# Kernel tuning notes

Measured on AMD Instinct MI355X. Metric: run time of the kernel, lower is better.

The kernel has to match this reference:

```python
import jax, jax.numpy as jnp
import numpy as np

D_MODEL = 1024
N_HEADS = 16
CHUNK_LEN = 50
MEM_LEN = 16
TOTAL_PROB = 20000
TOTAL_SKILL = 1000
B = 64
L = 2000
EPS = 1e-5


def _layernorm(x, g, b):
    mu = jnp.mean(x, axis=-1, keepdims=True)
    var = jnp.var(x, axis=-1, keepdims=True)
    return (x - mu) * jax.lax.rsqrt(var + EPS) * g + b


def setup_inputs() -> dict:
    key = jax.random.key(0)
    ks = jax.random.split(key, 20)
    s = 0.02
    D = D_MODEL
    emb_problem = (jax.random.normal(ks[0], (TOTAL_PROB, D), jnp.float32) * s).at[0].set(0.0)  # padding_idx=0
    emb_skill = (jax.random.normal(ks[1], (TOTAL_SKILL, D), jnp.float32) * s).at[0].set(0.0)
    mem_init = jax.random.normal(ks[2], (1, MEM_LEN, D), jnp.float32) * s
    pos_emb = jax.random.normal(ks[3], (MEM_LEN + CHUNK_LEN, D), jnp.float32) * s
    w_qkv = jax.random.normal(ks[4], (3 * D, D), jnp.float32) * s
    b_qkv = jnp.zeros((3 * D,), jnp.float32)
    w_out = jax.random.normal(ks[5], (D, D), jnp.float32) * s
    b_out = jnp.zeros((D,), jnp.float32)
    w1 = jax.random.normal(ks[6], (4 * D, D), jnp.float32) * s
    b1 = jnp.zeros((4 * D,), jnp.float32)
    w2 = jax.random.normal(ks[7], (D, 4 * D), jnp.float32) * s
    b2 = jnp.zeros((D,), jnp.float32)
    g_attn = jnp.ones((D,), jnp.float32)
    be_attn = jnp.zeros((D,), jnp.float32)
    g_ffn = jnp.ones((D,), jnp.float32)
    be_ffn = jnp.zeros((D,), jnp.float32)
    w_gate = jax.random.normal(ks[8], (D, D), jnp.float32) * s
    b_gate = jnp.zeros((D,), jnp.float32)
    in_prob = jax.random.randint(ks[9], (B, L), 0, TOTAL_PROB, dtype=jnp.int64 if jax.config.jax_enable_x64 else jnp.int32)
    in_skill = jax.random.randint(ks[10], (B, L), 0, TOTAL_SKILL, dtype=jnp.int64 if jax.config.jax_enable_x64 else jnp.int32)
    return dict(in_prob=in_prob, in_skill=in_skill, emb_problem=emb_problem, emb_skill=emb_skill,
                mem_init=mem_init, pos_emb=pos_emb, w_qkv=w_qkv, b_qkv=b_qkv, w_out=w_out, b_out=b_out,
                w1=w1, b1=b1, w2=w2, b2=b2, g_attn=g_attn, be_attn=be_attn, g_ffn=g_ffn, be_ffn=be_ffn,
                w_gate=w_gate, b_gate=b_gate)


def _mha(z, w_qkv, b_qkv, w_out, b_out, mask):
    # z: [B, T, D]; mask: [T, T] bool, True = disallowed (torch attn_mask semantics)
    Bz, T, D = z.shape
    dh = D // N_HEADS
    qkv = z @ w_qkv.T + b_qkv  # [B, T, 3D]
    q, k, v = jnp.split(qkv, 3, axis=-1)
    def heads(x):
        return x.reshape(Bz, T, N_HEADS, dh).transpose(0, 2, 1, 3)  # [B, H, T, dh]
    q, k, v = heads(q), heads(k), heads(v)
    scores = jnp.einsum('bhqd,bhkd->bhqk', q, k) / jnp.sqrt(jnp.float32(dh))
    scores = jnp.where(mask[None, None], jnp.float32(-1e9), scores)
    a = jax.nn.softmax(scores, axis=-1)
    o = jnp.einsum('bhqk,bhkd->bhqd', a, v)  # [B, H, T, dh]
    o = o.transpose(0, 2, 1, 3).reshape(Bz, T, D)
    return o @ w_out.T + b_out


def reference(in_prob, in_skill, emb_problem, emb_skill, mem_init, pos_emb,
              w_qkv, b_qkv, w_out, b_out, w1, b1, w2, b2,
              g_attn, be_attn, g_ffn, be_ffn, w_gate, b_gate):
    Bx, Lx = in_prob.shape
    D = emb_problem.shape[1]
    x = emb_problem[in_prob] + emb_skill[in_skill]  # [B, L, D]
    n_chunks = Lx // CHUNK_LEN
    T = MEM_LEN + CHUNK_LEN
    # block mask: memory fully visible, chunk part strictly causal
    causal = jnp.triu(jnp.ones((CHUNK_LEN, CHUNK_LEN), bool), k=1)
    mask = jnp.zeros((T, T), bool).at[MEM_LEN:, MEM_LEN:].set(causal)
    pos = pos_emb[:T][None]  # [1, T, D]
    chunks = x.reshape(Bx, n_chunks, CHUNK_LEN, D).transpose(1, 0, 2, 3)  # [K, B, Lc, D]
    mem0 = jnp.broadcast_to(mem_init, (Bx, MEM_LEN, D))

    def step(mem, xs):
        chunk, kidx = xs
        z = jnp.concatenate([mem, chunk], axis=1) + pos  # [B, T, D]
        z = z + _mha(_layernorm(z, g_attn, be_attn), w_qkv, b_qkv, w_out, b_out, mask)
        h = _layernorm(z, g_ffn, be_ffn)
        z = z + (jax.nn.relu(h @ w1.T + b1) @ w2.T + b2)
        mem_cand = z[:, :MEM_LEN]
        h_k = z[:, MEM_LEN:]
        g = jax.nn.sigmoid(mem_cand @ w_gate.T + b_gate)
        mem_gated = g * mem_cand + (1.0 - g) * mem
        mem_new = jnp.where(kidx == 0, mem_cand, mem_gated)  # first chunk: no gate
        return mem_new, h_k

    mem_final, hs = jax.lax.scan(step, mem0, (chunks, jnp.arange(n_chunks)))
    enc_out = hs.transpose(1, 0, 2, 3).reshape(Bx, Lx, D)
    return enc_out, mem_final
```

## Files before the change

### kernel.cpp

```cpp
#include <hip/hip_runtime.h>
#include <hip/hip_bf16.h>

#define D_MODEL 1024
#define N_HEADS 16
#define DH 64
#define CHUNK_LEN 50
#define MEM_LEN 16
#define TT 66
#define BB 64
#define LL 2000
#define NCHUNK 40
#define MTOK (BB*TT)

typedef _Float16 half8_t __attribute__((ext_vector_type(8)));
typedef __attribute__((ext_vector_type(4))) float f32x4;

typedef __attribute__((address_space(1))) const void GVoid;
typedef __attribute__((address_space(3))) void LVoid;

__device__ __forceinline__ void gload16(const void* g, void* l) {
  __builtin_amdgcn_global_load_lds((GVoid*)g, (LVoid*)l, 16, 0, 0);
}

__global__ __launch_bounds__(256) void f2h_kernel(const float* __restrict__ in,
                                                  _Float16* __restrict__ out, int n) {
  int i = (blockIdx.x * 256 + threadIdx.x) * 4;
  if (i < n) {
    float4 v = *(const float4*)(in + i);
    out[i+0] = (_Float16)v.x;
    out[i+1] = (_Float16)v.y;
    out[i+2] = (_Float16)v.z;
    out[i+3] = (_Float16)v.w;
  }
}

__global__ __launch_bounds__(256) void build_z_ln(
    const int* __restrict__ in_prob, const int* __restrict__ in_skill,
    const float* __restrict__ emb_p, const float* __restrict__ emb_s,
    const float* __restrict__ mem_src, int mem_bstride,
    const float* __restrict__ pos,
    const float* __restrict__ gam, const float* __restrict__ bet,
    float* __restrict__ z, _Float16* __restrict__ zn, int chunk)
{
  int row = blockIdx.x;
  int b = row / TT, t = row % TT;
  int tid = threadIdx.x;
  int d = tid * 4;
  float4 v;
  if (t < MEM_LEN) {
    v = *(const float4*)(mem_src + (size_t)b*mem_bstride + t*D_MODEL + d);
  } else {
    int tok = chunk*CHUNK_LEN + (t - MEM_LEN);
    int p = in_prob[b*LL + tok];
    int s = in_skill[b*LL + tok];
    float4 vp = *(const float4*)(emb_p + (size_t)p*D_MODEL + d);
    float4 vs = *(const float4*)(emb_s + (size_t)s*D_MODEL + d);
    v = make_float4(vp.x+vs.x, vp.y+vs.y, vp.z+vs.z, vp.w+vs.w);
  }
  float4 pv = *(const float4*)(pos + t*D_MODEL + d);
  v.x += pv.x; v.y += pv.y; v.z += pv.z; v.w += pv.w;
  *(float4*)(z + (size_t)row*D_MODEL + d) = v;
  float sum = v.x+v.y+v.z+v.w;
  float sq  = v.x*v.x+v.y*v.y+v.z*v.z+v.w*v.w;
  #pragma unroll
  for (int off = 32; off; off >>= 1) {
    sum += __shfl_down(sum, off, 64);
    sq  += __shfl_down(sq,  off, 64);
  }
  __shared__ float rs_[4], rq_[4];
  int wave = tid >> 6, lane = tid & 63;
  if (lane == 0) { rs_[wave] = sum; rq_[wave] = sq; }
  __syncthreads();
  sum = rs_[0]+rs_[1]+rs_[2]+rs_[3];
  sq  = rq_[0]+rq_[1]+rq_[2]+rq_[3];
  float mu  = sum * (1.0f/D_MODEL);
  float var = sq  * (1.0f/D_MODEL) - mu*mu;
  float rstd = rsqrtf(var + 1e-5f);
  float4 gv = *(const float4*)(gam + d);
  float4 bv = *(const float4*)(bet + d);
  _Float16* o = zn + (size_t)row*D_MODEL + d;
  o[0] = (_Float16)((v.x-mu)*rstd*gv.x + bv.x);
  o[1] = (_Float16)((v.y-mu)*rstd*gv.y + bv.y);
  o[2] = (_Float16)((v.z-mu)*rstd*gv.z + bv.z);
  o[3] = (_Float16)((v.w-mu)*rstd*gv.w + bv.w);
}

__global__ __launch_bounds__(256) void ln_kernel(
    const float* __restrict__ z, const float* __restrict__ gam, const float* __restrict__ bet,
    _Float16* __restrict__ out)
{
  int row = blockIdx.x;
  int tid = threadIdx.x;
  int d = tid * 4;
  float4 v = *(const float4*)(z + (size_t)row*D_MODEL + d);
  float sum = v.x+v.y+v.z+v.w;
  float sq  = v.x*v.x+v.y*v.y+v.z*v.z+v.w*v.w;
  #pragma unroll
  for (int off = 32; off; off >>= 1) {
    sum += __shfl_down(sum, off, 64);
    sq  += __shfl_down(sq,  off, 64);
  }
  __shared__ float rs_[4], rq_[4];
  int wave = tid >> 6, lane = tid & 63;
  if (lane == 0) { rs_[wave] = sum; rq_[wave] = sq; }
  __syncthreads();
  sum = rs_[0]+rs_[1]+rs_[2]+rs_[3];
  sq  = rq_[0]+rq_[1]+rq_[2]+rq_[3];
  float mu  = sum * (1.0f/D_MODEL);
  float var = sq  * (1.0f/D_MODEL) - mu*mu;
  float rstd = rsqrtf(var + 1e-5f);
  float4 gv = *(const float4*)(gam + d);
  float4 bv = *(const float4*)(bet + d);
  _Float16* o = out + (size_t)row*D_MODEL + d;
  o[0] = (_Float16)((v.x-mu)*rstd*gv.x + bv.x);
  o[1] = (_Float16)((v.y-mu)*rstd*gv.y + bv.y);
  o[2] = (_Float16)((v.z-mu)*rstd*gv.z + bv.z);
  o[3] = (_Float16)((v.w-mu)*rstd*gv.w + bv.w);
}

__global__ __launch_bounds__(256) void attn_kernel(
    const _Float16* __restrict__ qkv, _Float16* __restrict__ attn_o)
{
  __shared__ float qs_t[64*68 + 8];
  __shared__ float ks_t[64*68 + 8];
  __shared__ float vs[TT*DH];
  __shared__ float sc[TT*67];
  int bh = blockIdx.x; int b = bh >> 4, h = bh & 15;
  int tid = threadIdx.x;
  const _Float16* base = qkv + (size_t)b*TT*3072 + h*DH;
  for (int i = tid; i < TT*DH; i += 256) {
    int t = i >> 6, d2 = i & 63;
    const _Float16* rp = base + (size_t)t*3072 + d2;
    qs_t[d2*68 + t] = (float)rp[0];
    ks_t[d2*68 + t] = (float)rp[1024];
    vs[t*64 + d2]   = (float)rp[2048];
  }
  __syncthreads();
  if (tid < 153) {
    int ti = tid / 9, tj = tid % 9;
    int qi0 = ti*4, kj0 = tj*8;
    float acc[4][8];
    #pragma unroll
    for (int i = 0; i < 4; i++)
      #pragma unroll
      for (int j = 0; j < 8; j++) acc[i][j] = 0.f;
    for (int d2 = 0; d2 < 64; d2++) {
      float4 qv = *(const float4*)(qs_t + d2*68 + qi0);
      float4 k0 = *(const float4*)(ks_t + d2*68 + kj0);
      float4 k1 = *(const float4*)(ks_t + d2*68 + kj0 + 4);
      float q_[4] = {qv.x, qv.y, qv.z, qv.w};
      float k_[8] = {k0.x, k0.y, k0.z, k0.w, k1.x, k1.y, k1.z, k1.w};
      #pragma unroll
      for (int i = 0; i < 4; i++)
        #pragma unroll
        for (int j = 0; j < 8; j++)
          acc[i][j] += q_[i]*k_[j];
    }
    #pragma unroll
    for (int i = 0; i < 4; i++) {
      int qi = qi0 + i;
      if (qi >= TT) continue;
      #pragma unroll
      for (int j = 0; j < 8; j++) {
        int kj = kj0 + j;
        if (kj >= TT) continue;
        float s;
        if (qi >= MEM_LEN && kj >= MEM_LEN && kj > qi) s = -1e9f;
        else s = acc[i][j]*0.125f;
        sc[qi*67 + kj] = s;
      }
    }
  }
  __syncthreads();
  if (tid < TT) {
    float* r = sc + tid*67;
    float m = -1e30f;
    for (int j = 0; j < TT; j++) m = fmaxf(m, r[j]);
    float ssum = 0.f;
    for (int j = 0; j < TT; j++) { float e = __expf(r[j]-m); r[j] = e; ssum += e; }
    float inv = 1.f/ssum;
    for (int j = 0; j < TT; j++) r[j] *= inv;
  }
  __syncthreads();
  if (tid < 136) {
    int ti = tid >> 3, tj = tid & 7;
    int qi0 = ti*4, d20 = tj*8;
    float acc[4][8];
    #pragma unroll
    for (int i = 0; i < 4; i++)
      #pragma unroll
      for (int j = 0; j < 8; j++) acc[i][j] = 0.f;
    for (int kj = 0; kj < TT; kj++) {
      float a_[4];
      #pragma unroll
      for (int i = 0; i < 4; i++)
        a_[i] = (qi0 + i < TT) ? sc[(qi0+i)*67 + kj] : 0.f;
      float4 v0 = *(const float4*)(vs + kj*64 + d20);
      float4 v1 = *(const float4*)(vs + kj*64 + d20 + 4);
      float v_[8] = {v0.x, v0.y, v0.z, v0.w, v1.x, v1.y, v1.z, v1.w};
      #pragma unroll
      for (int i = 0; i < 4; i++)
        #pragma unroll
        for (int j = 0; j < 8; j++)
          acc[i][j] += a_[i]*v_[j];
    }
    #pragma unroll
    for (int i = 0; i < 4; i++) {
      int qi = qi0 + i;
      if (qi >= TT) continue;
      _Float16* o = attn_o + ((size_t)b*TT + qi)*D_MODEL + h*DH + d20;
      #pragma unroll
      for (int j = 0; j < 8; j++) o[j] = (_Float16)acc[i][j];
    }
  }
}

__global__ __launch_bounds__(256) void finalize_reduce(
    const float* __restrict__ z, const float* __restrict__ p0, const float* __restrict__ p1,
    const float* __restrict__ b2,
    float* __restrict__ enc_out, float* __restrict__ mem,
    _Float16* __restrict__ mcb, float* __restrict__ mcf, int chunk)
{
  int row = blockIdx.x; int b = row / TT, t = row % TT;
  int d = threadIdx.x * 4;
  size_t idx = (size_t)row*D_MODEL + d;
  float4 v  = *(const float4*)(z  + idx);
  float4 a0 = *(const float4*)(p0 + idx);
  float4 a1 = *(const float4*)(p1 + idx);
  float4 bv = *(const float4*)(b2 + d);
  v.x += a0.x + a1.x + bv.x;
  v.y += a0.y + a1.y + bv.y;
  v.z += a0.z + a1.z + bv.z;
  v.w += a0.w + a1.w + bv.w;
  if (t >= MEM_LEN) {
    size_t o = ((size_t)b*LL + chunk*CHUNK_LEN + (t - MEM_LEN))*D_MODEL + d;
    *(float4*)(enc_out + o) = v;
  } else {
    size_t mrow = (size_t)b*MEM_LEN + t;
    if (chunk == 0) {
      *(float4*)(mem + mrow*D_MODEL + d) = v;
    } else {
      *(float4*)(mcf + mrow*D_MODEL + d) = v;
      _Float16* o = mcb + mrow*D_MODEL + d;
      o[0] = (_Float16)v.x;
      o[1] = (_Float16)v.y;
      o[2] = (_Float16)v.z;
      o[3] = (_Float16)v.w;
    }
  }
}

__global__ __launch_bounds__(256) void copy_mem_kernel(const float* __restrict__ mem,
                                                       float* __restrict__ out) {
  int i = (blockIdx.x * 256 + threadIdx.x) * 4;
  float4 v = *(const float4*)(mem + i);
  *(float4*)(out + i) = v;
}

#define EPI_QKV   0
#define EPI_RESID 1
#define EPI_RELU  2
#define EPI_PART  3

#define KSLICE 2048

template<int EPI>
__global__ __launch_bounds__(256) void gemm_bt(
    const _Float16* __restrict__ A,
    const _Float16* __restrict__ Bw,
    const float* __restrict__ bias,
    float* __restrict__ zres,
    _Float16* __restrict__ obf,
    float* __restrict__ p1,
    int K, int lda, int ldo)
{
  __shared__ short As[2][128*32];
  __shared__ short Bs[2][128*32];
  int tid = threadIdx.x;
  int lane = tid & 63, wave = tid >> 6;
  int wr = wave >> 1, wc = wave & 1;
  int tm = blockIdx.y * 128, tn = blockIdx.x * 128;
  f32x4 acc[4][4] = {};
  const short* Ash = (const short*)A;
  const short* Bsh = (const short*)Bw;
  if constexpr (EPI == EPI_PART) {
    Ash += (size_t)blockIdx.z * KSLICE;
    Bsh += (size_t)blockIdx.z * KSLICE;
  }
  int e0 = tid * 8;
  int r0 = e0 >> 5, c0 = e0 & 31;
  int c0s = c0 ^ (((r0 >> 1) & 3) << 3);
  int ko = (lane >> 4) * 8;
  int rr = lane & 15;
  int swz = ((rr >> 1) & 3) << 3;

  auto STAGE = [&](int buf, int kt) {
    gload16(Ash + (size_t)(tm +      r0)*lda + kt + c0s, (char*)&As[buf][0] +        wave*1024);
    gload16(Ash + (size_t)(tm + 64 + r0)*lda + kt + c0s, (char*)&As[buf][0] + 4096 + wave*1024);
    gload16(Bsh + (size_t)(tn +      r0)*lda + kt + c0s, (char*)&Bs[buf][0] +        wave*1024);
    gload16(Bsh + (size_t)(tn + 64 + r0)*lda + kt + c0s, (char*)&Bs[buf][0] + 4096 + wave*1024);
  };
  auto COMPUTE = [&](int buf) {
    half8_t af[4], bfr[4];
    int kos = ko ^ swz;
    #pragma unroll
    for (int m = 0; m < 4; m++)
      af[m] = *(const half8_t*)(&As[buf][(wr*64 + m*16 + rr)*32 + kos]);
    #pragma unroll
    for (int n = 0; n < 4; n++)
      bfr[n] = *(const half8_t*)(&Bs[buf][(wc*64 + n*16 + rr)*32 + kos]);
    #pragma unroll
    for (int m = 0; m < 4; m++)
      #pragma unroll
      for (int n = 0; n < 4; n++)
        acc[m][n] = __builtin_amdgcn_mfma_f32_16x16x32_f16(af[m], bfr[n], acc[m][n], 0, 0, 0);
  };

  STAGE(0, 0);
  int cur = 0;
  for (int kt = 32; kt < K; kt += 32) {
    STAGE(cur ^ 1, kt);
    asm volatile("s_waitcnt vmcnt(4)" ::: "memory");
    __builtin_amdgcn_s_barrier();
    COMPUTE(cur);
    asm volatile("" ::: "memory");
    __builtin_amdgcn_s_barrier();
    cur ^= 1;
  }
  asm volatile("s_waitcnt vmcnt(0)" ::: "memory");
  __builtin_amdgcn_s_barrier();
  COMPUTE(cur);

  int rbase = tm + wr*64 + ((lane >> 4) << 2);
  int cbase = tn + wc*64 + (lane & 15);
  float* pp = nullptr;
  if constexpr (EPI == EPI_PART) pp = (blockIdx.z == 0) ? zres : p1;
  #pragma unroll
  for (int n = 0; n < 4; n++) {
    int col = cbase + n*16;
    float bs = (EPI == EPI_PART) ? 0.f : bias[col];
    #pragma unroll
    for (int m = 0; m < 4; m++) {
      #pragma unroll
      for (int i = 0; i < 4; i++) {
        int r = rbase + m*16 + i;
        float v = acc[m][n][i] + bs;
        if constexpr (EPI == EPI_QKV) {
          obf[(size_t)r*ldo + col] = (_Float16)v;
        } else if constexpr (EPI == EPI_RESID) {
          zres[(size_t)r*D_MODEL + col] += v;
        } else if constexpr (EPI == EPI_RELU) {
          obf[(size_t)r*ldo + col] = (_Float16)fmaxf(v, 0.f);
        } else {
          pp[(size_t)r*D_MODEL + col] = v;
        }
      }
    }
  }
}

__global__ __launch_bounds__(256) void gemm_gate64(
    const _Float16* __restrict__ A,
    const _Float16* __restrict__ Bw,
    const float* __restrict__ bias,
    const float* __restrict__ mcf,
    float* __restrict__ mem)
{
  __shared__ short As[64*32];
  __shared__ short Bs[64*32];
  int tid = threadIdx.x;
  int lane = tid & 63, wave = tid >> 6;
  int wr = wave >> 1, wc = wave & 1;
  int tm = blockIdx.y * 64, tn = blockIdx.x * 64;
  f32x4 acc[2][2] = {};
  const short* Ash = (const short*)A;
  const short* Bsh = (const short*)Bw;
  int e0 = tid * 8;
  int r0 = e0 >> 5, c0 = e0 & 31;

  for (int kt = 0; kt < 1024; kt += 32) {
    gload16(Ash + (size_t)(tm + r0)*1024 + kt + c0, (char*)As + wave*1024);
    gload16(Bsh + (size_t)(tn + r0)*1024 + kt + c0, (char*)Bs + wave*1024);
    __syncthreads();
    half8_t af[2], bfr[2];
    int ko = (lane >> 4) * 8;
    int rr = lane & 15;
    #pragma unroll
    for (int m = 0; m < 2; m++)
      af[m] = *(const half8_t*)(As + (wr*32 + m*16 + rr)*32 + ko);
    #pragma unroll
    for (int n = 0; n < 2; n++)
      bfr[n] = *(const half8_t*)(Bs + (wc*32 + n*16 + rr)*32 + ko);
    #pragma unroll
    for (int m = 0; m < 2; m++)
      #pragma unroll
      for (int n = 0; n < 2; n++)
        acc[m][n] = __builtin_amdgcn_mfma_f32_16x16x32_f16(af[m], bfr[n], acc[m][n], 0, 0, 0);
    __syncthreads();
  }

  int rbase = tm + wr*32 + ((lane >> 4) << 2);
  int cbase = tn + wc*32 + (lane & 15);
  #pragma unroll
  for (int n = 0; n < 2; n++) {
    int col = cbase + n*16;
    float bs = bias[col];
    #pragma unroll
    for (int m = 0; m < 2; m++) {
      #pragma unroll
      for (int i = 0; i < 4; i++) {
        int r = rbase + m*16 + i;
        float g = 1.f / (1.f + __expf(-(acc[m][n][i] + bs)));
        size_t mi = (size_t)r*D_MODEL + col;
        mem[mi] = g*mcf[mi] + (1.f - g)*mem[mi];
      }
    }
  }
}

extern "C" void kernel_launch(void* const* d_in, const int* in_sizes, int n_in,
                              void* d_out, int out_size, void* d_ws, size_t ws_size,
                              hipStream_t stream) {
  const int*   in_prob  = (const int*)d_in[0];
  const int*   in_skill = (const int*)d_in[1];
  const float* emb_p    = (const float*)d_in[2];
  const float* emb_s    = (const float*)d_in[3];
  const float* mem_init = (const float*)d_in[4];
  const float* pos      = (const float*)d_in[5];
  const float* w_qkv    = (const float*)d_in[6];
  const float* b_qkv    = (const float*)d_in[7];
  const float* w_out    = (const float*)d_in[8];
  const float* b_out    = (const float*)d_in[9];
  const float* w1       = (const float*)d_in[10];
  const float* b1       = (const float*)d_in[11];
  const float* w2       = (const float*)d_in[12];
  const float* b2       = (const float*)d_in[13];
  const float* g_attn   = (const float*)d_in[14];
  const float* be_attn  = (const float*)d_in[15];
  const float* g_ffn    = (const float*)d_in[16];
  const float* be_ffn   = (const float*)d_in[17];
  const float* w_gate   = (const float*)d_in[18];
  const float* b_gate   = (const float*)d_in[19];

  float* enc_out = (float*)d_out;
  float* mem_out = enc_out + (size_t)BB*LL*D_MODEL;

  char* ws = (char*)d_ws;
  size_t off = 0;
  auto alloc = [&](size_t bytes) -> char* {
    char* p = ws + off;
    off += (bytes + 255) & ~(size_t)255;
    return p;
  };
  _Float16* wqkv_h = (_Float16*)alloc((size_t)3072*1024*2);
  _Float16* wout_h = (_Float16*)alloc((size_t)1024*1024*2);
  _Float16* w1_h   = (_Float16*)alloc((size_t)4096*1024*2);
  _Float16* w2_h   = (_Float16*)alloc((size_t)1024*4096*2);
  _Float16* wgate_h= (_Float16*)alloc((size_t)1024*1024*2);
  float*    z      = (float*)alloc((size_t)MTOK*D_MODEL*4);
  _Float16* zn     = (_Float16*)alloc((size_t)MTOK*D_MODEL*2);
  _Float16* qkv    = (_Float16*)alloc((size_t)MTOK*3072*2);
  _Float16* ao     = (_Float16*)alloc((size_t)MTOK*D_MODEL*2);
  _Float16* hb     = (_Float16*)alloc((size_t)MTOK*D_MODEL*2);
  _Float16* fh     = (_Float16*)alloc((size_t)MTOK*4096*2);
  _Float16* mcb    = (_Float16*)alloc((size_t)1024*1024*2);
  float*    mem    = (float*)alloc((size_t)1024*1024*4);
  float*    mcf    = (float*)alloc((size_t)1024*1024*4);
  float*    part0  = (float*)alloc((size_t)MTOK*D_MODEL*4);
  float*    part1  = (float*)alloc((size_t)MTOK*D_MODEL*4);
  if (off > ws_size) return;

  f2h_kernel<<<(3072*1024)/1024, 256, 0, stream>>>(w_qkv, wqkv_h, 3072*1024);
  f2h_kernel<<<(1024*1024)/1024, 256, 0, stream>>>(w_out, wout_h, 1024*1024);
  f2h_kernel<<<(4096*1024)/1024, 256, 0, stream>>>(w1, w1_h, 4096*1024);
  f2h_kernel<<<(1024*4096)/1024, 256, 0, stream>>>(w2, w2_h, 1024*4096);
  f2h_kernel<<<(1024*1024)/1024, 256, 0, stream>>>(w_gate, wgate_h, 1024*1024);

  for (int c = 0; c < NCHUNK; c++) {
    const float* msrc = (c == 0) ? mem_init : mem;
    int mbs = (c == 0) ? 0 : MEM_LEN*D_MODEL;
    build_z_ln<<<MTOK, 256, 0, stream>>>(in_prob, in_skill, emb_p, emb_s,
                                         msrc, mbs, pos, g_attn, be_attn, z, zn, c);
    gemm_bt<EPI_QKV><<<dim3(3072/128, MTOK/128), 256, 0, stream>>>(
        zn, wqkv_h, b_qkv, nullptr, qkv, nullptr, 1024, 1024, 3072);
    attn_kernel<<<BB*N_HEADS, 256, 0, stream>>>(qkv, ao);
    gemm_bt<EPI_RESID><<<dim3(1024/128, MTOK/128), 256, 0, stream>>>(
        ao, wout_h, b_out, z, nullptr, nullptr, 1024, 1024, 1024);
    ln_kernel<<<MTOK, 256, 0, stream>>>(z, g_ffn, be_ffn, hb);
    gemm_bt<EPI_RELU><<<dim3(4096/128, MTOK/128), 256, 0, stream>>>(
        hb, w1_h, b1, nullptr, fh, nullptr, 1024, 1024, 4096);
    gemm_bt<EPI_PART><<<dim3(1024/128, MTOK/128, 2), 256, 0, stream>>>(
        fh, w2_h, b2, part0, nullptr, part1, KSLICE, 4096, 1024);
    finalize_reduce<<<MTOK, 256, 0, stream>>>(z, part0, part1, b2,
                                              enc_out, mem, mcb, mcf, c);
    if (c > 0) {
      gemm_gate64<<<dim3(1024/64, 1024/64), 256, 0, stream>>>(
          mcb, wgate_h, b_gate, mcf, mem);
    }
  }
  copy_mem_kernel<<<(1024*1024)/1024, 256, 0, stream>>>(mem, mem_out);
}
```

Baseline: 11.55 ms.

## Hoist chunk-token QKV projection out of recurrence; triple-buffer GEMM pipeline

Result: slower. 12.32 ms (+6.6%).

```diff
diff --git a/kernel.cpp b/kernel.cpp
--- a/kernel.cpp
+++ b/kernel.cpp
@@ -85,6 +85,49 @@
   o[3] = (_Float16)((v.w-mu)*rstd*gv.w + bv.w);
 }
 
+__global__ __launch_bounds__(256) void build_z_ln_all(
+    const int* __restrict__ in_prob, const int* __restrict__ in_skill,
+    const float* __restrict__ emb_p, const float* __restrict__ emb_s,
+    const float* __restrict__ pos,
+    const float* __restrict__ gam, const float* __restrict__ bet,
+    _Float16* __restrict__ zn_all)
+{
+  int row = blockIdx.x;
+  int tok = row % LL;
+  int t = MEM_LEN + (tok % CHUNK_LEN);
+  int tid = threadIdx.x;
+  int d = tid * 4;
+  int p = in_prob[row];
+  int s = in_skill[row];
+  float4 vp = *(const float4*)(emb_p + (size_t)p*D_MODEL + d);
+  float4 vs = *(const float4*)(emb_s + (size_t)s*D_MODEL + d);
+  float4 pv = *(const float4*)(pos + t*D_MODEL + d);
+  float4 v = make_float4(vp.x+vs.x+pv.x, vp.y+vs.y+pv.y, vp.z+vs.z+pv.z, vp.w+vs.w+pv.w);
+  float sum = v.x+v.y+v.z+v.w;
+  float sq  = v.x*v.x+v.y*v.y+v.z*v.z+v.w*v.w;
+  #pragma unroll
+  for (int off = 32; off; off >>= 1) {
+    sum += __shfl_down(sum, off, 64);
+    sq  += __shfl_down(sq,  off, 64);
+  }
+  __shared__ float rs_[4], rq_[4];
+  int wave = tid >> 6, lane = tid & 63;
+  if (lane == 0) { rs_[wave] = sum; rq_[wave] = sq; }
+  __syncthreads();
+  sum = rs_[0]+rs_[1]+rs_[2]+rs_[3];
+  sq  = rq_[0]+rq_[1]+rq_[2]+rq_[3];
+  float mu  = sum * (1.0f/D_MODEL);
+  float var = sq  * (1.0f/D_MODEL) - mu*mu;
+  float rstd = rsqrtf(var + 1e-5f);
+  float4 gv = *(const float4*)(gam + d);
+  float4 bv = *(const float4*)(bet + d);
+  _Float16* o = zn_all + (size_t)row*D_MODEL + d;
+  o[0] = (_Float16)((v.x-mu)*rstd*gv.x + bv.x);
+  o[1] = (_Float16)((v.y-mu)*rstd*gv.y + bv.y);
+  o[2] = (_Float16)((v.z-mu)*rstd*gv.z + bv.z);
+  o[3] = (_Float16)((v.w-mu)*rstd*gv.w + bv.w);
+}
+
 __global__ __launch_bounds__(256) void ln_kernel(
     const float* __restrict__ z, const float* __restrict__ gam, const float* __restrict__ bet,
     _Float16* __restrict__ out)
@@ -119,7 +162,9 @@
 }
 
 __global__ __launch_bounds__(256) void attn_kernel(
-    const _Float16* __restrict__ qkv, _Float16* __restrict__ attn_o)
+    const _Float16* __restrict__ baseM, int strideMb,
+    const _Float16* __restrict__ baseC, int strideCb, int offC,
+    _Float16* __restrict__ attn_o)
 {
   __shared__ float qs_t[64*68 + 8];
   __shared__ float ks_t[64*68 + 8];
@@ -127,10 +172,11 @@
   __shared__ float sc[TT*67];
   int bh = blockIdx.x; int b = bh >> 4, h = bh & 15;
   int tid = threadIdx.x;
-  const _Float16* base = qkv + (size_t)b*TT*3072 + h*DH;
   for (int i = tid; i < TT*DH; i += 256) {
     int t = i >> 6, d2 = i & 63;
-    const _Float16* rp = base + (size_t)t*3072 + d2;
+    const _Float16* rp;
+    if (t < MEM_LEN) rp = baseM + ((size_t)b*strideMb + t)*3072 + h*DH + d2;
+    else             rp = baseC + ((size_t)b*strideCb + offC + (t - MEM_LEN))*3072 + h*DH + d2;
     qs_t[d2*68 + t] = (float)rp[0];
     ks_t[d2*68 + t] = (float)rp[1024];
     vs[t*64 + d2]   = (float)rp[2048];
@@ -264,7 +310,7 @@
 
 #define KSLICE 2048
 
-template<int EPI>
+template<int EPI, int AMAP = 0>
 __global__ __launch_bounds__(256) void gemm_bt(
     const _Float16* __restrict__ A,
     const _Float16* __restrict__ Bw,
@@ -274,8 +320,8 @@
     float* __restrict__ p1,
     int K, int lda, int ldo)
 {
-  __shared__ short As[2][128*32];
-  __shared__ short Bs[2][128*32];
+  __shared__ short As[3][128*32];
+  __shared__ short Bs[3][128*32];
   int tid = threadIdx.x;
   int lane = tid & 63, wave = tid >> 6;
   int wr = wave >> 1, wc = wave & 1;
@@ -294,9 +340,13 @@
   int rr = lane & 15;
   int swz = ((rr >> 1) & 3) << 3;
 
+  auto arow = [&](int r) -> size_t {
+    if constexpr (AMAP) return (size_t)((r >> 4) * TT + (r & 15));
+    else return (size_t)r;
+  };
   auto STAGE = [&](int buf, int kt) {
-    gload16(Ash + (size_t)(tm +      r0)*lda + kt + c0s, (char*)&As[buf][0] +        wave*1024);
-    gload16(Ash + (size_t)(tm + 64 + r0)*lda + kt + c0s, (char*)&As[buf][0] + 4096 + wave*1024);
+    gload16(Ash + arow(tm +      r0)*lda + kt + c0s, (char*)&As[buf][0] +        wave*1024);
+    gload16(Ash + arow(tm + 64 + r0)*lda + kt + c0s, (char*)&As[buf][0] + 4096 + wave*1024);
     gload16(Bsh + (size_t)(tn +      r0)*lda + kt + c0s, (char*)&Bs[buf][0] +        wave*1024);
     gload16(Bsh + (size_t)(tn + 64 + r0)*lda + kt + c0s, (char*)&Bs[buf][0] + 4096 + wave*1024);
   };
@@ -317,34 +367,43 @@
   };
 
   STAGE(0, 0);
-  int cur = 0;
-  for (int kt = 32; kt < K; kt += 32) {
-    STAGE(cur ^ 1, kt);
-    asm volatile("s_waitcnt vmcnt(4)" ::: "memory");
+  STAGE(1, 32);
+  int n = K >> 5;
+  int sb = 2, cb = 0;
+  for (int i = 0; i < n - 2; i++) {
+    STAGE(sb, (i + 2) << 5);
+    asm volatile("s_waitcnt vmcnt(8)" ::: "memory");
     __builtin_amdgcn_s_barrier();
-    COMPUTE(cur);
-    asm volatile("" ::: "memory");
+    COMPUTE(cb);
+    asm volatile("s_waitcnt lgkmcnt(0)" ::: "memory");
     __builtin_amdgcn_s_barrier();
-    cur ^= 1;
-  }
+    sb = (sb == 2) ? 0 : sb + 1;
+    cb = (cb == 2) ? 0 : cb + 1;
+  }
+  asm volatile("s_waitcnt vmcnt(4)" ::: "memory");
+  __builtin_amdgcn_s_barrier();
+  COMPUTE(cb);
+  asm volatile("s_waitcnt lgkmcnt(0)" ::: "memory");
+  __builtin_amdgcn_s_barrier();
+  cb = (cb == 2) ? 0 : cb + 1;
   asm volatile("s_waitcnt vmcnt(0)" ::: "memory");
   __builtin_amdgcn_s_barrier();
-  COMPUTE(cur);
+  COMPUTE(cb);
 
   int rbase = tm + wr*64 + ((lane >> 4) << 2);
   int cbase = tn + wc*64 + (lane & 15);
   float* pp = nullptr;
   if constexpr (EPI == EPI_PART) pp = (blockIdx.z == 0) ? zres : p1;
   #pragma unroll
-  for (int n = 0; n < 4; n++) {
-    int col = cbase + n*16;
+  for (int nn = 0; nn < 4; nn++) {
+    int col = cbase + nn*16;
     float bs = (EPI == EPI_PART) ? 0.f : bias[col];
     #pragma unroll
     for (int m = 0; m < 4; m++) {
       #pragma unroll
       for (int i = 0; i < 4; i++) {
         int r = rbase + m*16 + i;
-        float v = acc[m][n][i] + bs;
+        float v = acc[m][nn][i] + bs;
         if constexpr (EPI == EPI_QKV) {
           obf[(size_t)r*ldo + col] = (_Float16)v;
         } else if constexpr (EPI == EPI_RESID) {
@@ -468,7 +527,12 @@
   float*    mcf    = (float*)alloc((size_t)1024*1024*4);
   float*    part0  = (float*)alloc((size_t)MTOK*D_MODEL*4);
   float*    part1  = (float*)alloc((size_t)MTOK*D_MODEL*4);
-  if (off > ws_size) return;
+  size_t base_off = off;
+  if (base_off > ws_size) return;
+
+  _Float16* zn_all  = (_Float16*)alloc((size_t)BB*LL*D_MODEL*2);
+  _Float16* qkv_all = (_Float16*)alloc((size_t)BB*LL*3072*2);
+  bool pre = (off <= ws_size);
 
   f2h_kernel<<<(3072*1024)/1024, 256, 0, stream>>>(w_qkv, wqkv_h, 3072*1024);
   f2h_kernel<<<(1024*1024)/1024, 256, 0, stream>>>(w_out, wout_h, 1024*1024);
@@ -476,14 +540,27 @@
   f2h_kernel<<<(1024*4096)/1024, 256, 0, stream>>>(w2, w2_h, 1024*4096);
   f2h_kernel<<<(1024*1024)/1024, 256, 0, stream>>>(w_gate, wgate_h, 1024*1024);
 
+  if (pre) {
+    build_z_ln_all<<<BB*LL, 256, 0, stream>>>(in_prob, in_skill, emb_p, emb_s,
+                                              pos, g_attn, be_attn, zn_all);
+    gemm_bt<EPI_QKV><<<dim3(3072/128, (BB*LL)/128), 256, 0, stream>>>(
+        zn_all, wqkv_h, b_qkv, nullptr, qkv_all, nullptr, 1024, 1024, 3072);
+  }
+
   for (int c = 0; c < NCHUNK; c++) {
     const float* msrc = (c == 0) ? mem_init : mem;
     int mbs = (c == 0) ? 0 : MEM_LEN*D_MODEL;
     build_z_ln<<<MTOK, 256, 0, stream>>>(in_prob, in_skill, emb_p, emb_s,
                                          msrc, mbs, pos, g_attn, be_attn, z, zn, c);
-    gemm_bt<EPI_QKV><<<dim3(3072/128, MTOK/128), 256, 0, stream>>>(
-        zn, wqkv_h, b_qkv, nullptr, qkv, nullptr, 1024, 1024, 3072);
-    attn_kernel<<<BB*N_HEADS, 256, 0, stream>>>(qkv, ao);
+    if (pre) {
+      gemm_bt<EPI_QKV, 1><<<dim3(3072/128, 1024/128), 256, 0, stream>>>(
+          zn, wqkv_h, b_qkv, nullptr, qkv, nullptr, 1024, 1024, 3072);
+      attn_kernel<<<BB*N_HEADS, 256, 0, stream>>>(qkv, MEM_LEN, qkv_all, LL, c*CHUNK_LEN, ao);
+    } else {
+      gemm_bt<EPI_QKV><<<dim3(3072/128, MTOK/128), 256, 0, stream>>>(
+          zn, wqkv_h, b_qkv, nullptr, qkv, nullptr, 1024, 1024, 3072);
+      attn_kernel<<<BB*N_HEADS, 256, 0, stream>>>(qkv, TT, qkv, TT, MEM_LEN, ao);
+    }
     gemm_bt<EPI_RESID><<<dim3(1024/128, MTOK/128), 256, 0, stream>>>(
         ao, wout_h, b_out, z, nullptr, nullptr, 1024, 1024, 1024);
     ln_kernel<<<MTOK, 256, 0, stream>>>(z, g_ffn, be_ffn, hb);
```

## Hoist chunk-token work out of recurrent loop; only memory rows stay sequential

Applied to the files above, without the earlier changes.

After: 11.74 ms. Within noise of the previous version (+1.6%).

```diff
diff --git a/kernel.cpp b/kernel.cpp
--- a/kernel.cpp
+++ b/kernel.cpp
@@ -11,6 +11,7 @@
 #define LL 2000
 #define NCHUNK 40
 #define MTOK (BB*TT)
+#define MROW (BB*MEM_LEN)
 
 typedef _Float16 half8_t __attribute__((ext_vector_type(8)));
 typedef __attribute__((ext_vector_type(4))) float f32x4;
@@ -32,6 +33,33 @@
     out[i+2] = (_Float16)v.z;
     out[i+3] = (_Float16)v.w;
   }
+}
+
+__device__ __forceinline__ void ln_row(float4 v, int tid, int d,
+                                       const float* gam, const float* bet,
+                                       _Float16* o) {
+  float sum = v.x+v.y+v.z+v.w;
+  float sq  = v.x*v.x+v.y*v.y+v.z*v.z+v.w*v.w;
+  #pragma unroll
+  for (int off = 32; off; off >>= 1) {
+    sum += __shfl_down(sum, off, 64);
+    sq  += __shfl_down(sq,  off, 64);
+  }
+  __shared__ float rs_[4], rq_[4];
+  int wave = tid >> 6, lane = tid & 63;
+  if (lane == 0) { rs_[wave] = sum; rq_[wave] = sq; }
+  __syncthreads();
+  sum = rs_[0]+rs_[1]+rs_[2]+rs_[3];
+  sq  = rq_[0]+rq_[1]+rq_[2]+rq_[3];
+  float mu  = sum * (1.0f/D_MODEL);
+  float var = sq  * (1.0f/D_MODEL) - mu*mu;
+  float rstd = rsqrtf(var + 1e-5f);
+  float4 gv = *(const float4*)(gam + d);
+  float4 bv = *(const float4*)(bet + d);
+  o[0] = (_Float16)((v.x-mu)*rstd*gv.x + bv.x);
+  o[1] = (_Float16)((v.y-mu)*rstd*gv.y + bv.y);
+  o[2] = (_Float16)((v.z-mu)*rstd*gv.z + bv.z);
+  o[3] = (_Float16)((v.w-mu)*rstd*gv.w + bv.w);
 }
 
 __global__ __launch_bounds__(256) void build_z_ln(
@@ -60,29 +88,48 @@
   float4 pv = *(const float4*)(pos + t*D_MODEL + d);
   v.x += pv.x; v.y += pv.y; v.z += pv.z; v.w += pv.w;
   *(float4*)(z + (size_t)row*D_MODEL + d) = v;
-  float sum = v.x+v.y+v.z+v.w;
-  float sq  = v.x*v.x+v.y*v.y+v.z*v.z+v.w*v.w;
-  #pragma unroll
-  for (int off = 32; off; off >>= 1) {
-    sum += __shfl_down(sum, off, 64);
-    sq  += __shfl_down(sq,  off, 64);
-  }
-  __shared__ float rs_[4], rq_[4];
-  int wave = tid >> 6, lane = tid & 63;
-  if (lane == 0) { rs_[wave] = sum; rq_[wave] = sq; }
-  __syncthreads();
-  sum = rs_[0]+rs_[1]+rs_[2]+rs_[3];
-  sq  = rq_[0]+rq_[1]+rq_[2]+rq_[3];
-  float mu  = sum * (1.0f/D_MODEL);
-  float var = sq  * (1.0f/D_MODEL) - mu*mu;
-  float rstd = rsqrtf(var + 1e-5f);
-  float4 gv = *(const float4*)(gam + d);
-  float4 bv = *(const float4*)(bet + d);
-  _Float16* o = zn + (size_t)row*D_MODEL + d;
-  o[0] = (_Float16)((v.x-mu)*rstd*gv.x + bv.x);
-  o[1] = (_Float16)((v.y-mu)*rstd*gv.y + bv.y);
-  o[2] = (_Float16)((v.z-mu)*rstd*gv.z + bv.z);
-  o[3] = (_Float16)((v.w-mu)*rstd*gv.w + bv.w);
+  ln_row(v, tid, d, gam, bet, zn + (size_t)row*D_MODEL + d);
+}
+
+__global__ __launch_bounds__(256) void build_z_ln_mem(
+    const float* __restrict__ mem_src, int mem_bstride,
+    const float* __restrict__ pos,
+    const float* __restrict__ gam, const float* __restrict__ bet,
+    float* __restrict__ z, _Float16* __restrict__ zn)
+{
+  int row = blockIdx.x;
+  int b = row >> 4, t = row & 15;
+  int tid = threadIdx.x;
+  int d = tid * 4;
+  float4 v = *(const float4*)(mem_src + (size_t)b*mem_bstride + t*D_MODEL + d);
+  float4 pv = *(const float4*)(pos + t*D_MODEL + d);
+  v.x += pv.x; v.y += pv.y; v.z += pv.z; v.w += pv.w;
+  *(float4*)(z + (size_t)row*D_MODEL + d) = v;
+  ln_row(v, tid, d, gam, bet, zn + (size_t)row*D_MODEL + d);
+}
+
+__global__ __launch_bounds__(256) void build_z_all(
+    const int* __restrict__ in_prob, const int* __restrict__ in_skill,
+    const float* __restrict__ emb_p, const float* __restrict__ emb_s,
+    const float* __restrict__ pos,
+    const float* __restrict__ gam, const float* __restrict__ bet,
+    _Float16* __restrict__ z16_all, _Float16* __restrict__ zn_all)
+{
+  int row = blockIdx.x;
+  int tok = row % LL;
+  int t = MEM_LEN + (tok % CHUNK_LEN);
+  int tid = threadIdx.x;
+  int d = tid * 4;
+  int p = in_prob[row];
+  int s = in_skill[row];
+  float4 vp = *(const float4*)(emb_p + (size_t)p*D_MODEL + d);
+  float4 vs = *(const float4*)(emb_s + (size_t)s*D_MODEL + d);
+  float4 pv = *(const float4*)(pos + t*D_MODEL + d);
+  float4 v = make_float4(vp.x+vs.x, vp.y+vs.y, vp.z+vs.z, vp.w+vs.w);
+  v.x += pv.x; v.y += pv.y; v.z += pv.z; v.w += pv.w;
+  _Float16* zo = z16_all + (size_t)row*D_MODEL + d;
+  zo[0] = (_Float16)v.x; zo[1] = (_Float16)v.y; zo[2] = (_Float16)v.z; zo[3] = (_Float16)v.w;
+  ln_row(v, tid, d, gam, bet, zn_all + (size_t)row*D_MODEL + d);
 }
 
 __global__ __launch_bounds__(256) void ln_kernel(
@@ -93,33 +140,14 @@
   int tid = threadIdx.x;
   int d = tid * 4;
   float4 v = *(const float4*)(z + (size_t)row*D_MODEL + d);
-  float sum = v.x+v.y+v.z+v.w;
-  float sq  = v.x*v.x+v.y*v.y+v.z*v.z+v.w*v.w;
-  #pragma unroll
-  for (int off = 32; off; off >>= 1) {
-    sum += __shfl_down(sum, off, 64);
-    sq  += __shfl_down(sq,  off, 64);
-  }
-  __shared__ float rs_[4], rq_[4];
-  int wave = tid >> 6, lane = tid & 63;
-  if (lane == 0) { rs_[wave] = sum; rq_[wave] = sq; }
-  __syncthreads();
-  sum = rs_[0]+rs_[1]+rs_[2]+rs_[3];
-  sq  = rq_[0]+rq_[1]+rq_[2]+rq_[3];
-  float mu  = sum * (1.0f/D_MODEL);
-  float var = sq  * (1.0f/D_MODEL) - mu*mu;
-  float rstd = rsqrtf(var + 1e-5f);
-  float4 gv = *(const float4*)(gam + d);
-  float4 bv = *(const float4*)(bet + d);
-  _Float16* o = out + (size_t)row*D_MODEL + d;
-  o[0] = (_Float16)((v.x-mu)*rstd*gv.x + bv.x);
-  o[1] = (_Float16)((v.y-mu)*rstd*gv.y + bv.y);
-  o[2] = (_Float16)((v.z-mu)*rstd*gv.z + bv.z);
-  o[3] = (_Float16)((v.w-mu)*rstd*gv.w + bv.w);
+  ln_row(v, tid, d, gam, bet, out + (size_t)row*D_MODEL + d);
 }
 
 __global__ __launch_bounds__(256) void attn_kernel(
-    const _Float16* __restrict__ qkv, _Float16* __restrict__ attn_o)
+    const _Float16* __restrict__ qM, int sM,
+    const _Float16* __restrict__ qC, int sC, int oC,
+    _Float16* __restrict__ aM, int saM,
+    _Float16* __restrict__ aC, int saC, int oaC)
 {
   __shared__ float qs_t[64*68 + 8];
   __shared__ float ks_t[64*68 + 8];
@@ -127,10 +155,11 @@
   __shared__ float sc[TT*67];
   int bh = blockIdx.x; int b = bh >> 4, h = bh & 15;
   int tid = threadIdx.x;
-  const _Float16* base = qkv + (size_t)b*TT*3072 + h*DH;
   for (int i = tid; i < TT*DH; i += 256) {
     int t = i >> 6, d2 = i & 63;
-    const _Float16* rp = base + (size_t)t*3072 + d2;
+    const _Float16* rp;
+    if (t < MEM_LEN) rp = qM + ((size_t)b*sM + t)*3072 + h*DH + d2;
+    else             rp = qC + ((size_t)b*sC + oC + (t - MEM_LEN))*3072 + h*DH + d2;
     qs_t[d2*68 + t] = (float)rp[0];
     ks_t[d2*68 + t] = (float)rp[1024];
     vs[t*64 + d2]   = (float)rp[2048];
@@ -208,7 +237,9 @@
     for (int i = 0; i < 4; i++) {
       int qi = qi0 + i;
       if (qi >= TT) continue;
-      _Float16* o = attn_o + ((size_t)b*TT + qi)*D_MODEL + h*DH + d20;
+      _Float16* o;
+      if (qi < MEM_LEN) o = aM + ((size_t)b*saM + qi)*D_MODEL + h*DH + d20;
+      else              o = aC + ((size_t)b*saC + oaC + (qi - MEM_LEN))*D_MODEL + h*DH + d20;
       #pragma unroll
       for (int j = 0; j < 8; j++) o[j] = (_Float16)acc[i][j];
     }
@@ -242,11 +273,33 @@
     } else {
       *(float4*)(mcf + mrow*D_MODEL + d) = v;
       _Float16* o = mcb + mrow*D_MODEL + d;
-      o[0] = (_Float16)v.x;
-      o[1] = (_Float16)v.y;
-      o[2] = (_Float16)v.z;
-      o[3] = (_Float16)v.w;
-    }
+      o[0] = (_Float16)v.x; o[1] = (_Float16)v.y; o[2] = (_Float16)v.z; o[3] = (_Float16)v.w;
+    }
+  }
+}
+
+__global__ __launch_bounds__(256) void finalize_mem(
+    const float* __restrict__ z, const float* __restrict__ p0, const float* __restrict__ p1,
+    const float* __restrict__ b2,
+    float* __restrict__ mem, _Float16* __restrict__ mcb, float* __restrict__ mcf, int chunk)
+{
+  int row = blockIdx.x;
+  int d = threadIdx.x * 4;
+  size_t idx = (size_t)row*D_MODEL + d;
+  float4 v  = *(const float4*)(z  + idx);
+  float4 a0 = *(const float4*)(p0 + idx);
+  float4 a1 = *(const float4*)(p1 + idx);
+  float4 bv = *(const float4*)(b2 + d);
+  v.x += a0.x + a1.x + bv.x;
+  v.y += a0.y + a1.y + bv.y;
+  v.z += a0.z + a1.z + bv.z;
+  v.w += a0.w + a1.w + bv.w;
+  if (chunk == 0) {
+    *(float4*)(mem + idx) = v;
+  } else {
+    *(float4*)(mcf + idx) = v;
+    _Float16* o = mcb + idx;
+    o[0] = (_Float16)v.x; o[1] = (_Float16)v.y; o[2] = (_Float16)v.z; o[3] = (_Float16)v.w;
   }
 }
 
@@ -257,10 +310,13 @@
   *(float4*)(out + i) = v;
 }
 
-#define EPI_QKV   0
-#define EPI_RESID 1
-#define EPI_RELU  2
-#define EPI_PART  3
+#define EPI_QKV     0
+#define EPI_RESID   1
+#define EPI_RELU    2
+#define EPI_PART    3
+#define EPI_RESID16 4
+#define EPI_ENC     5
+#define EPI_GATE    6
 
 #define KSLICE 2048
 
@@ -292,7 +348,7 @@
   int c0s = c0 ^ (((r0 >> 1) & 3) << 3);
   int ko = (lane >> 4) * 8;
   int rr = lane & 15;
-  int swz = ((rr >> 1) & 3) << 3;
+  int kos = ko ^ (((rr >> 1) & 3) << 3);
 
   auto STAGE = [&](int buf, int kt) {
     gload16(Ash + (size_t)(tm +      r0)*lda + kt + c0s, (char*)&As[buf][0] +        wave*1024);
@@ -302,7 +358,6 @@
   };
   auto COMPUTE = [&](int buf) {
     half8_t af[4], bfr[4];
-    int kos = ko ^ swz;
     #pragma unroll
     for (int m = 0; m < 4; m++)
       af[m] = *(const half8_t*)(&As[buf][(wr*64 + m*16 + rr)*32 + kos]);
@@ -336,38 +391,45 @@
   float* pp = nullptr;
   if constexpr (EPI == EPI_PART) pp = (blockIdx.z == 0) ? zres : p1;
   #pragma unroll
-  for (int n = 0; n < 4; n++) {
-    int col = cbase + n*16;
+  for (int nn = 0; nn < 4; nn++) {
+    int col = cbase + nn*16;
     float bs = (EPI == EPI_PART) ? 0.f : bias[col];
     #pragma unroll
     for (int m = 0; m < 4; m++) {
       #pragma unroll
       for (int i = 0; i < 4; i++) {
         int r = rbase + m*16 + i;
-        float v = acc[m][n][i] + bs;
+        float v = acc[m][nn][i] + bs;
         if constexpr (EPI == EPI_QKV) {
           obf[(size_t)r*ldo + col] = (_Float16)v;
         } else if constexpr (EPI == EPI_RESID) {
           zres[(size_t)r*D_MODEL + col] += v;
         } else if constexpr (EPI == EPI_RELU) {
           obf[(size_t)r*ldo + col] = (_Float16)fmaxf(v, 0.f);
-        } else {
+        } else if constexpr (EPI == EPI_PART) {
           pp[(size_t)r*D_MODEL + col] = v;
+        } else if constexpr (EPI == EPI_RESID16) {
+          zres[(size_t)r*D_MODEL + col] = (float)obf[(size_t)r*D_MODEL + col] + v;
+        } else if constexpr (EPI == EPI_ENC) {
+          p1[(size_t)r*D_MODEL + col] = zres[(size_t)r*D_MODEL + col] + v;
         }
       }
     }
   }
 }
 
-__global__ __launch_bounds__(256) void gemm_gate64(
+template<int EPI>
+__global__ __launch_bounds__(256) void gemm64(
     const _Float16* __restrict__ A,
     const _Float16* __restrict__ Bw,
     const float* __restrict__ bias,
-    const float* __restrict__ mcf,
-    float* __restrict__ mem)
-{
-  __shared__ short As[64*32];
-  __shared__ short Bs[64*32];
+    float* __restrict__ zres,
+    _Float16* __restrict__ obf,
+    float* __restrict__ p1,
+    int K, int lda, int ldo)
+{
+  __shared__ short As[2][64*32];
+  __shared__ short Bs[2][64*32];
   int tid = threadIdx.x;
   int lane = tid & 63, wave = tid >> 6;
   int wr = wave >> 1, wc = wave & 1;
@@ -375,44 +437,75 @@
   f32x4 acc[2][2] = {};
   const short* Ash = (const short*)A;
   const short* Bsh = (const short*)Bw;
-  int e0 = tid * 8;
-  int r0 = e0 >> 5, c0 = e0 & 31;
-
-  for (int kt = 0; kt < 1024; kt += 32) {
-    gload16(Ash + (size_t)(tm + r0)*1024 + kt + c0, (char*)As + wave*1024);
-    gload16(Bsh + (size_t)(tn + r0)*1024 + kt + c0, (char*)Bs + wave*1024);
-    __syncthreads();
+  if constexpr (EPI == EPI_PART) {
+    Ash += (size_t)blockIdx.z * KSLICE;
+    Bsh += (size_t)blockIdx.z * KSLICE;
+  }
+  int r0 = tid >> 2, c0 = (tid & 3) * 8;
+  int c0s = c0 ^ (((r0 >> 1) & 3) << 3);
+  int ko = (lane >> 4) * 8;
+  int rr = lane & 15;
+  int kos = ko ^ (((rr >> 1) & 3) << 3);
+
+  auto STAGE = [&](int buf, int kt) {
+    gload16(Ash + (size_t)(tm + r0)*lda + kt + c0s, (char*)&As[buf][0] + wave*1024);
+    gload16(Bsh + (size_t)(tn + r0)*lda + kt + c0s, (char*)&Bs[buf][0] + wave*1024);
+  };
+  auto COMPUTE = [&](int buf) {
     half8_t af[2], bfr[2];
-    int ko = (lane >> 4) * 8;
-    int rr = lane & 15;
     #pragma unroll
     for (int m = 0; m < 2; m++)
-      af[m] = *(const half8_t*)(As + (wr*32 + m*16 + rr)*32 + ko);
+      af[m] = *(const half8_t*)(&As[buf][(wr*32 + m*16 + rr)*32 + kos]);
     #pragma unroll
     for (int n = 0; n < 2; n++)
-      bfr[n] = *(const half8_t*)(Bs + (wc*32 + n*16 + rr)*32 + ko);
+      bfr[n] = *(const half8_t*)(&Bs[buf][(wc*32 + n*16 + rr)*32 + kos]);
     #pragma unroll
     for (int m = 0; m < 2; m++)
       #pragma unroll
       for (int n = 0; n < 2; n++)
         acc[m][n] = __builtin_amdgcn_mfma_f32_16x16x32_f16(af[m], bfr[n], acc[m][n], 0, 0, 0);
-    __syncthreads();
-  }
+  };
+
+  STAGE(0, 0);
+  int cur = 0;
+  for (int kt = 32; kt < K; kt += 32) {
+    STAGE(cur ^ 1, kt);
+    asm volatile("s_waitcnt vmcnt(2)" ::: "memory");
+    __builtin_amdgcn_s_barrier();
+    COMPUTE(cur);
+    asm volatile("" ::: "memory");
+    __builtin_amdgcn_s_barrier();
+    cur ^= 1;
+  }
+  asm volatile("s_waitcnt vmcnt(0)" ::: "memory");
+  __builtin_amdgcn_s_barrier();
+  COMPUTE(cur);
 
   int rbase = tm + wr*32 + ((lane >> 4) << 2);
   int cbase = tn + wc*32 + (lane & 15);
+  float* pp = nullptr;
+  if constexpr (EPI == EPI_PART) pp = (blockIdx.z == 0) ? zres : p1;
   #pragma unroll
-  for (int n = 0; n < 2; n++) {
-    int col = cbase + n*16;
-    float bs = bias[col];
+  for (int nn = 0; nn < 2; nn++) {
+    int col = cbase + nn*16;
+    float bs = (EPI == EPI_PART) ? 0.f : bias[col];
     #pragma unroll
     for (int m = 0; m < 2; m++) {
       #pragma unroll
       for (int i = 0; i < 4; i++) {
         int r = rbase + m*16 + i;
-        float g = 1.f / (1.f + __expf(-(acc[m][n][i] + bs)));
-        size_t mi = (size_t)r*D_MODEL + col;
-        mem[mi] = g*mcf[mi] + (1.f - g)*mem[mi];
+        float v = acc[m][nn][i] + bs;
+        if constexpr (EPI == EPI_QKV) {
+          obf[(size_t)r*ldo + col] = (_Float16)v;
+        } else if constexpr (EPI == EPI_RESID) {
+          zres[(size_t)r*D_MODEL + col] += v;
+        } else if constexpr (EPI == EPI_PART) {
+          pp[(size_t)r*D_MODEL + col] = v;
+        } else if constexpr (EPI == EPI_GATE) {
+          float g = 1.f / (1.f + __expf(-v));
+          size_t mi = (size_t)r*D_MODEL + col;
+          p1[mi] = g*zres[mi] + (1.f - g)*p1[mi];
+        }
       }
     }
   }
@@ -463,12 +556,19 @@
   _Float16* ao     = (_Float16*)alloc((size_t)MTOK*D_MODEL*2);
   _Float16* hb     = (_Float16*)alloc((size_t)MTOK*D_MODEL*2);
   _Float16* fh     = (_Float16*)alloc((size_t)MTOK*4096*2);
-  _Float16* mcb    = (_Float16*)alloc((size_t)1024*1024*2);
-  float*    mem    = (float*)alloc((size_t)1024*1024*4);
-  float*    mcf    = (float*)alloc((size_t)1024*1024*4);
+  _Float16* mcb    = (_Float16*)alloc((size_t)MROW*D_MODEL*2);
+  float*    mem    = (float*)alloc((size_t)MROW*D_MODEL*4);
+  float*    mcf    = (float*)alloc((size_t)MROW*D_MODEL*4);
   float*    part0  = (float*)alloc((size_t)MTOK*D_MODEL*4);
   float*    part1  = (float*)alloc((size_t)MTOK*D_MODEL*4);
   if (off > ws_size) return;
+
+  const size_t MALL = (size_t)BB*LL;
+  _Float16* zn_all  = (_Float16*)alloc(MALL*D_MODEL*2);
+  _Float16* z16_all = (_Float16*)alloc(MALL*D_MODEL*2);
+  _Float16* qkv_all = (_Float16*)alloc(MALL*3072*2);
+  _Float16* fh_g    = (_Float16*)alloc((MALL/4)*4096*2);
+  bool pre = (off <= ws_size);
 
   f2h_kernel<<<(3072*1024)/1024, 256, 0, stream>>>(w_qkv, wqkv_h, 3072*1024);
   f2h_kernel<<<(1024*1024)/1024, 256, 0, stream>>>(w_out, wout_h, 1024*1024);
@@ -476,27 +576,74 @@
   f2h_kernel<<<(1024*4096)/1024, 256, 0, stream>>>(w2, w2_h, 1024*4096);
   f2h_kernel<<<(1024*1024)/1024, 256, 0, stream>>>(w_gate, wgate_h, 1024*1024);
 
-  for (int c = 0; c < NCHUNK; c++) {
-    const float* msrc = (c == 0) ? mem_init : mem;
-    int mbs = (c == 0) ? 0 : MEM_LEN*D_MODEL;
-    build_z_ln<<<MTOK, 256, 0, stream>>>(in_prob, in_skill, emb_p, emb_s,
-                                         msrc, mbs, pos, g_attn, be_attn, z, zn, c);
-    gemm_bt<EPI_QKV><<<dim3(3072/128, MTOK/128), 256, 0, stream>>>(
-        zn, wqkv_h, b_qkv, nullptr, qkv, nullptr, 1024, 1024, 3072);
-    attn_kernel<<<BB*N_HEADS, 256, 0, stream>>>(qkv, ao);
-    gemm_bt<EPI_RESID><<<dim3(1024/128, MTOK/128), 256, 0, stream>>>(
-        ao, wout_h, b_out, z, nullptr, nullptr, 1024, 1024, 1024);
-    ln_kernel<<<MTOK, 256, 0, stream>>>(z, g_ffn, be_ffn, hb);
-    gemm_bt<EPI_RELU><<<dim3(4096/128, MTOK/128), 256, 0, stream>>>(
-        hb, w1_h, b1, nullptr, fh, nullptr, 1024, 1024, 4096);
-    gemm_bt<EPI_PART><<<dim3(1024/128, MTOK/128, 2), 256, 0, stream>>>(
-        fh, w2_h, b2, part0, nullptr, part1, KSLICE, 4096, 1024);
-    finalize_reduce<<<MTOK, 256, 0, stream>>>(z, part0, part1, b2,
-                                              enc_out, mem, mcb, mcf, c);
-    if (c > 0) {
-      gemm_gate64<<<dim3(1024/64, 1024/64), 256, 0, stream>>>(
-          mcb, wgate_h, b_gate, mcf, mem);
-    }
-  }
-  copy_mem_kernel<<<(1024*1024)/1024, 256, 0, stream>>>(mem, mem_out);
-}
+  if (pre) {
+    _Float16* ao_all = zn_all;
+    float*    z1_all = (float*)qkv_all;
+    _Float16* hb_all = z16_all;
+
+    build_z_all<<<(int)MALL, 256, 0, stream>>>(in_prob, in_skill, emb_p, emb_s,
+                                               pos, g_attn, be_attn, z16_all, zn_all);
+    gemm_bt<EPI_QKV><<<dim3(3072/128, MALL/128), 256, 0, stream>>>(
+        zn_all, wqkv_h, b_qkv, nullptr, qkv_all, nullptr, 1024, 1024, 3072);
+
+    for (int c = 0; c < NCHUNK; c++) {
+      const float* msrc = (c == 0) ? mem_init : mem;
+      int mbs = (c == 0) ? 0 : MEM_LEN*D_MODEL;
+      build_z_ln_mem<<<MROW, 256, 0, stream>>>(msrc, mbs, pos, g_attn, be_attn, z, zn);
+      gemm64<EPI_QKV><<<dim3(3072/64, MROW/64), 256, 0, stream>>>(
+          zn, wqkv_h, b_qkv, nullptr, qkv, nullptr, 1024, 1024, 3072);
+      attn_kernel<<<BB*N_HEADS, 256, 0, stream>>>(
+          qkv, MEM_LEN, qkv_all, LL, c*CHUNK_LEN,
+          ao, MEM_LEN, ao_all, LL, c*CHUNK_LEN);
+      gemm64<EPI_RESID><<<dim3(1024/64, MROW/64), 256, 0, stream>>>(
+          ao, wout_h, b_out, z, nullptr, nullptr, 1024, 1024, 1024);
+      ln_kernel<<<MROW, 256, 0, stream>>>(z, g_ffn, be_ffn, hb);
+      gemm_bt<EPI_RELU><<<dim3(4096/128, MROW/128), 256, 0, stream>>>(
+          hb, w1_h, b1, nullptr, fh, nullptr, 1024, 1024, 4096);
+      gemm64<EPI_PART><<<dim3(1024/64, MROW/64, 2), 256, 0, stream>>>(
+          fh, w2_h, nullptr, part0, nullptr, part1, KSLICE, 4096, 1024);
+      finalize_mem<<<MROW, 256, 0, stream>>>(z, part0, part1, b2, mem, mcb, mcf, c);
+      if (c > 0) {
+        gemm64<EPI_GATE><<<dim3(1024/64, MROW/64), 256, 0, stream>>>(
+            mcb, wgate_h, b_gate, mcf, nullptr, mem, 1024, 1024, 1024);
+      }
+    }
+
+    gemm_bt<EPI_RESID16><<<dim3(1024/128, MALL/128), 256, 0, stream>>>(
+        ao_all, wout_h, b_out, z1_all, z16_all, nullptr, 1024, 1024, 1024);
+    ln_kernel<<<(int)MALL, 256, 0, stream>>>(z1_all, g_ffn, be_ffn, hb_all);
+    const size_t MG = MALL / 4;
+    for (int g = 0; g < 4; g++) {
+      size_t r0 = (size_t)g * MG;
+      gemm_bt<EPI_RELU><<<dim3(4096/128, MG/128), 256, 0, stream>>>(
+          hb_all + r0*D_MODEL, w1_h, b1, nullptr, fh_g, nullptr, 1024, 1024, 4096);
+      gemm_bt<EPI_ENC><<<dim3(1024/128, MG/128), 256, 0, stream>>>(
+          fh_g, w2_h, b2, z1_all + r0*D_MODEL, nullptr, enc_out + r0*D_MODEL, 4096, 4096, 1024);
+    }
+  } else {
+    for (int c = 0; c < NCHUNK; c++) {
+      const float* msrc = (c == 0) ? mem_init : mem;
+      int mbs = (c == 0) ? 0 : MEM_LEN*D_MODEL;
+      build_z_ln<<<MTOK, 256, 0, stream>>>(in_prob, in_skill, emb_p, emb_s,
+                                           msrc, mbs, pos, g_attn, be_attn, z, zn, c);
+      gemm_bt<EPI_QKV><<<dim3(3072/128, MTOK/128), 256, 0, stream>>>(
+          zn, wqkv_h, b_qkv, nullptr, qkv, nullptr, 1024, 1024, 3072);
+      attn_kernel<<<BB*N_HEADS, 256, 0, stream>>>(
+          qkv, TT, qkv, TT, MEM_LEN, ao, TT, ao, TT, MEM_LEN);
+      gemm_bt<EPI_RESID><<<dim3(1024/128, MTOK/128), 256, 0, stream>>>(
+          ao, wout_h, b_out, z, nullptr, nullptr, 1024, 1024, 1024);
+      ln_kernel<<<MTOK, 256, 0, stream>>>(z, g_ffn, be_ffn, hb);
+      gemm_bt<EPI_RELU><<<dim3(4096/128, MTOK/128), 256, 0, stream>>>(
+          hb, w1_h, b1, nullptr, fh, nullptr, 1024, 1024, 4096);
+      gemm_bt<EPI_PART><<<dim3(1024/128, MTOK/128, 2), 256, 0, stream>>>(
+          fh, w2_h, nullptr, part0, nullptr, part1, KSLICE, 4096, 1024);
+      finalize_reduce<<<MTOK, 256, 0, stream>>>(z, part0, part1, b2,
+                                                enc_out, mem, mcb, mcf, c);
+      if (c > 0) {
+        gemm64<EPI_GATE><<<dim3(1024/64, MROW/64), 256, 0, stream>>>(
+            mcb, wgate_h, b_gate, mcf, nullptr, mem, 1024, 1024, 1024);
+      }
+    }
+  }
+  copy_mem_kernel<<<(MROW*D_MODEL)/1024, 256, 0, stream>>>(mem, mem_out);
+}
```
